# Optimization experiments

Hardware: AMD Instinct MI355X
Metric: run time of the kernel (lower is better)

Reference implementation:

```python
import jax, jax.numpy as jnp
import numpy as np

N = 25000      # nodes
E = 400000     # edges (avg degree 16)
D = 128        # input feature dim
H = 4          # heads in layer 1
O1 = 128       # per-head out dim layer 1
O2 = 64        # out dim layer 2 (1 head)
NG = 512       # number of graphs in batch
NEG_SLOPE = 0.2


def _gat_layer(x, src, dst, W, a_src, a_dst, bias, heads, out_dim):
    """PyG-style GATConv: gather, per-edge logits, segment softmax over dst, scatter-add."""
    n = x.shape[0]
    h = (x @ W).reshape(n, heads, out_dim)              # [N,H,O]
    al_s = jnp.sum(h * a_src, axis=-1)                  # [N,H]
    al_d = jnp.sum(h * a_dst, axis=-1)                  # [N,H]
    e = jax.nn.leaky_relu(al_s[src] + al_d[dst], NEG_SLOPE)   # [E,H]
    e_max = jax.ops.segment_max(e, dst, num_segments=n)        # [N,H]
    e_exp = jnp.exp(e - e_max[dst])
    denom = jax.ops.segment_sum(e_exp, dst, num_segments=n)    # [N,H]
    alpha = e_exp / denom[dst]                                  # [E,H]
    msg = alpha[:, :, None] * h[src]                             # [E,H,O]  (dominant traffic)
    out = jax.ops.segment_sum(msg, dst, num_segments=n)         # [N,H,O]
    return out.reshape(n, heads * out_dim) + bias


def setup_inputs() -> dict:
    key = jax.random.key(0)
    ks = jax.random.split(key, 16)
    x = jax.random.normal(ks[0], (N, D), dtype=jnp.float32)
    edge_index = jax.random.randint(ks[1], (2, E), 0, N, dtype=jnp.int64)
    batch = jnp.sort(jax.random.randint(ks[2], (N,), 0, NG, dtype=jnp.int64))
    def glorot(k, shape, fan_in):
        return jax.random.normal(k, shape, dtype=jnp.float32) * (1.0 / np.sqrt(fan_in))
    W1 = glorot(ks[3], (D, H * O1), D)
    a_src1 = glorot(ks[4], (H, O1), O1)
    a_dst1 = glorot(ks[5], (H, O1), O1)
    b1 = jnp.zeros((H * O1,), dtype=jnp.float32)
    W2 = glorot(ks[6], (H * O1, O2), H * O1)
    a_src2 = glorot(ks[7], (1, O2), O2)
    a_dst2 = glorot(ks[8], (1, O2), O2)
    b2 = jnp.zeros((O2,), dtype=jnp.float32)
    fc_w1 = glorot(ks[9], (O2, 32), O2)
    fc_b1 = jnp.zeros((32,), dtype=jnp.float32)
    fc_w2 = glorot(ks[10], (32, 1), 32)
    fc_b2 = jnp.zeros((1,), dtype=jnp.float32)
    return {"x": x, "edge_index": edge_index, "batch": batch,
            "W1": W1, "a_src1": a_src1, "a_dst1": a_dst1, "b1": b1,
            "W2": W2, "a_src2": a_src2, "a_dst2": a_dst2, "b2": b2,
            "fc_w1": fc_w1, "fc_b1": fc_b1, "fc_w2": fc_w2, "fc_b2": fc_b2}


def reference(x, edge_index, batch, W1, a_src1, a_dst1, b1, W2, a_src2, a_dst2, b2,
              fc_w1, fc_b1, fc_w2, fc_b2):
    n = x.shape[0]
    loop = jnp.arange(n, dtype=edge_index.dtype)
    src = jnp.concatenate([edge_index[0], loop])   # add_self_loops=True (PyG default)
    dst = jnp.concatenate([edge_index[1], loop])
    h1 = jax.nn.elu(_gat_layer(x, src, dst, W1, a_src1, a_dst1, b1, H, O1))   # [N, 512]
    h2 = jax.nn.elu(_gat_layer(h1, src, dst, W2, a_src2, a_dst2, b2, 1, O2))  # [N, 64]
    # global mean pool over graphs
    sums = jax.ops.segment_sum(h2, batch, num_segments=NG)                     # [NG, 64]
    cnt = jax.ops.segment_sum(jnp.ones((n,), dtype=h2.dtype), batch, num_segments=NG)
    pooled = sums / jnp.maximum(cnt, 1.0)[:, None]
    hid = jax.nn.relu(pooled @ fc_w1 + fc_b1)
    out = jax.nn.sigmoid(hid @ fc_w2 + fc_b2)
    return out.squeeze(-1)                                                     # [NG]
```

## Files before the change

kernel.cpp:

```cpp
#include <hip/hip_runtime.h>
#include <hip/hip_bf16.h>


typedef unsigned short u16;
typedef unsigned int u32;
typedef __attribute__((ext_vector_type(8))) short bf16x8;
typedef __attribute__((ext_vector_type(4))) float f32x4;

#define LRELU(v) ((v) > 0.0f ? (v) : 0.2f * (v))
#define ELU(v)   ((v) > 0.0f ? (v) : expm1f(v))

__device__ __forceinline__ u16 f2bf(float f) {
    union { float f; u32 u; } c; c.f = f;
    u32 u = c.u;
    u32 r = (u + 0x7fffu + ((u >> 16) & 1u)) >> 16;
    return (u16)r;
}
__device__ __forceinline__ float bf2f(u16 h) {
    return __uint_as_float(((u32)h) << 16);
}

__global__ __launch_bounds__(256) void prep_w(const float* __restrict__ W1,
                                              const float* __restrict__ W2,
                                              const float* __restrict__ a_s,
                                              const float* __restrict__ a_d,
                                              u16* __restrict__ W1f,
                                              u16* __restrict__ W2f,
                                              float* __restrict__ Wa) {
    int b = blockIdx.x;
    if (b < 384) {
        int idx = b * 256 + threadIdx.x;
        if (idx < 65536) {
            int fid = idx >> 9, l = (idx >> 3) & 63, j = idx & 7;
            int head = fid >> 5, cb = (fid >> 2) & 7, s = fid & 3;
            int col = head * 128 + cb * 16 + (l & 15);
            int k = s * 32 + 16 * (j >> 2) + 4 * (l >> 4) + (j & 3);
            W1f[idx] = f2bf(W1[(size_t)k * 512 + col]);
        } else {
            int i2 = idx - 65536;
            int fid = i2 >> 9, l = (i2 >> 3) & 63, j = i2 & 7;
            int c2 = fid >> 4, s = fid & 15;
            int col = c2 * 16 + (l & 15);
            int k = s * 32 + 16 * (j >> 2) + 4 * (l >> 4) + (j & 3);
            W2f[i2] = f2bf(W2[(size_t)k * 64 + col]);
        }
    } else {
        int idx = (b - 384) * 256 + threadIdx.x;
        int k = idx >> 3, j = idx & 7, h = j & 3;
        const float* a = (j < 4) ? (a_s + h * 128) : (a_d + h * 128);
        const float* wrow = W1 + (size_t)k * 512 + h * 128;
        float s = 0.f;
#pragma unroll 8
        for (int o = 0; o < 128; ++o) s += wrow[o] * a[o];
        Wa[k * 8 + j] = s;
    }
}

__global__ __launch_bounds__(256) void prep_x(const float* __restrict__ x,
                                              const float* __restrict__ Wa,
                                              u16* __restrict__ xbf,
                                              float* __restrict__ alS,
                                              float* __restrict__ alD, int Nn) {
    int lane = threadIdx.x & 63;
    int wave = threadIdx.x >> 6;
    float4 ls = *(const float4*)(Wa + lane * 8);
    float4 ld = *(const float4*)(Wa + lane * 8 + 4);
    float4 hs = *(const float4*)(Wa + (lane + 64) * 8);
    float4 hd = *(const float4*)(Wa + (lane + 64) * 8 + 4);
    int n = blockIdx.x * 4 + wave;
    if (n >= Nn) return;
    float x0 = x[(size_t)n * 128 + lane];
    float x1 = x[(size_t)n * 128 + lane + 64];
    xbf[(size_t)n * 128 + lane]      = f2bf(x0);
    xbf[(size_t)n * 128 + lane + 64] = f2bf(x1);
    float r0 = x0 * ls.x + x1 * hs.x;
    float r1 = x0 * ls.y + x1 * hs.y;
    float r2 = x0 * ls.z + x1 * hs.z;
    float r3 = x0 * ls.w + x1 * hs.w;
    float r4 = x0 * ld.x + x1 * hd.x;
    float r5 = x0 * ld.y + x1 * hd.y;
    float r6 = x0 * ld.z + x1 * hd.z;
    float r7 = x0 * ld.w + x1 * hd.w;
#pragma unroll
    for (int off = 32; off; off >>= 1) {
        r0 += __shfl_down(r0, off); r1 += __shfl_down(r1, off);
        r2 += __shfl_down(r2, off); r3 += __shfl_down(r3, off);
        r4 += __shfl_down(r4, off); r5 += __shfl_down(r5, off);
        r6 += __shfl_down(r6, off); r7 += __shfl_down(r7, off);
    }
    if (lane == 0) {
        *(float4*)(alS + (size_t)n * 4) = make_float4(r0, r1, r2, r3);
        *(float4*)(alD + (size_t)n * 4) = make_float4(r4, r5, r6, r7);
    }
}

__global__ __launch_bounds__(256) void count_kernel(const int* __restrict__ dst,
                                                    int E, int Nn, int* __restrict__ deg) {
    int e = blockIdx.x * 256 + threadIdx.x;
    if (e >= E + Nn) return;
    int d = (e < E) ? dst[e] : (e - E);
    atomicAdd(&deg[d], 1);
}

__global__ __launch_bounds__(256) void scanA_kernel(const int* __restrict__ deg,
                                                    int* __restrict__ offs,
                                                    int* __restrict__ bsum, int n) {
    __shared__ int sh[256];
    int b = blockIdx.x, t = threadIdx.x;
    int base = b * 2048 + t * 8;
    int v[8]; int s = 0;
#pragma unroll
    for (int j = 0; j < 8; ++j) { int i = base + j; v[j] = (i < n) ? deg[i] : 0; s += v[j]; }
    sh[t] = s;
    __syncthreads();
    for (int off = 1; off < 256; off <<= 1) {
        int u = (t >= off) ? sh[t - off] : 0;
        __syncthreads();
        sh[t] += u;
        __syncthreads();
    }
    int run = sh[t] - s;
    if (t == 255) bsum[b] = sh[255];
#pragma unroll
    for (int j = 0; j < 8; ++j) {
        run += v[j];
        int i = base + j;
        if (i < n) offs[i + 1] = run;
    }
}

__global__ __launch_bounds__(64) void scanB_kernel(int* __restrict__ bsum, int nb) {
    int t = threadIdx.x;
    int v = (t < nb) ? bsum[t] : 0;
#pragma unroll
    for (int off = 1; off < 64; off <<= 1) {
        int u = __shfl_up(v, off);
        if (t >= off) v += u;
    }
    if (t < nb) bsum[t] = v;
}

__global__ __launch_bounds__(256) void scanC_kernel(int* __restrict__ offs,
                                                    const int* __restrict__ bsum, int n) {
    int i = blockIdx.x * 256 + threadIdx.x;
    if (i == 0) offs[0] = 0;
    if (i >= n) return;
    int b = i >> 11;
    if (b > 0) offs[i + 1] += bsum[b - 1];
}

__global__ __launch_bounds__(256) void scatter_kernel(const int* __restrict__ src,
                                                      const int* __restrict__ dst,
                                                      int E, int Nn,
                                                      const int* __restrict__ offs,
                                                      int* __restrict__ fill,
                                                      const float* __restrict__ alS,
                                                      const float* __restrict__ alD,
                                                      int* __restrict__ sCSR,
                                                      int* __restrict__ dCSR,
                                                      float* __restrict__ wE1) {
    int e = blockIdx.x * 256 + threadIdx.x;
    if (e >= E + Nn) return;
    int s = (e < E) ? src[e] : (e - E);
    int d = (e < E) ? dst[e] : (e - E);
    int pos = offs[d] + atomicAdd(&fill[d], 1);
    sCSR[pos] = s;
    dCSR[pos] = d;
    float4 as = *(const float4*)(alS + (size_t)s * 4);
    float4 ad = *(const float4*)(alD + (size_t)d * 4);
    float4 w;
    float t;
    t = as.x + ad.x; w.x = expf(LRELU(t));
    t = as.y + ad.y; w.y = expf(LRELU(t));
    t = as.z + ad.z; w.z = expf(LRELU(t));
    t = as.w + ad.w; w.w = expf(LRELU(t));
    *(float4*)(wE1 + (size_t)pos * 4) = w;
}

__global__ __launch_bounds__(256) void aggx_kernel(const u16* __restrict__ xbf,
                                                   const int* __restrict__ sCSR,
                                                   const int* __restrict__ offs,
                                                   const float* __restrict__ wE,
                                                   u16* __restrict__ xaggF, int Nn) {
    int n = blockIdx.x * 4 + (threadIdx.x >> 6);
    int l = threadIdx.x & 63;
    if (n >= Nn) return;
    int half = l >> 5;
    int fl = (l & 31) * 4;
    float a0[4] = {0.f, 0.f, 0.f, 0.f};
    float a1[4] = {0.f, 0.f, 0.f, 0.f};
    float a2[4] = {0.f, 0.f, 0.f, 0.f};
    float a3[4] = {0.f, 0.f, 0.f, 0.f};
    float ws0 = 0.f, ws1 = 0.f, ws2 = 0.f, ws3 = 0.f;
    int s0 = offs[n], s1 = offs[n + 1];
    int i = s0 + half;
    for (; i + 6 < s1; i += 8) {
        int sn[4]; float4 w[4]; ushort4 u[4];
#pragma unroll
        for (int j = 0; j < 4; ++j) {
            int idx = i + 2 * j;
            sn[j] = sCSR[idx];
            w[j] = *(const float4*)(wE + (size_t)idx * 4);
        }
#pragma unroll
        for (int j = 0; j < 4; ++j)
            u[j] = *(const ushort4*)(xbf + (size_t)sn[j] * 128 + fl);
#pragma unroll
        for (int j = 0; j < 4; ++j) {
            float xv[4] = {bf2f(u[j].x), bf2f(u[j].y), bf2f(u[j].z), bf2f(u[j].w)};
#pragma unroll
            for (int q = 0; q < 4; ++q) {
                a0[q] += w[j].x * xv[q];
                a1[q] += w[j].y * xv[q];
                a2[q] += w[j].z * xv[q];
                a3[q] += w[j].w * xv[q];
            }
            ws0 += w[j].x; ws1 += w[j].y; ws2 += w[j].z; ws3 += w[j].w;
        }
    }
    for (; i < s1; i += 2) {
        int sn = sCSR[i];
        float4 w = *(const float4*)(wE + (size_t)i * 4);
        ushort4 u = *(const ushort4*)(xbf + (size_t)sn * 128 + fl);
        float xv[4] = {bf2f(u.x), bf2f(u.y), bf2f(u.z), bf2f(u.w)};
#pragma unroll
        for (int q = 0; q < 4; ++q) {
            a0[q] += w.x * xv[q];
            a1[q] += w.y * xv[q];
            a2[q] += w.z * xv[q];
            a3[q] += w.w * xv[q];
        }
        ws0 += w.x; ws1 += w.y; ws2 += w.z; ws3 += w.w;
    }
#pragma unroll
    for (int q = 0; q < 4; ++q) {
        a0[q] += __shfl_xor(a0[q], 32);
        a1[q] += __shfl_xor(a1[q], 32);
        a2[q] += __shfl_xor(a2[q], 32);
        a3[q] += __shfl_xor(a3[q], 32);
    }
    ws0 += __shfl_xor(ws0, 32); ws1 += __shfl_xor(ws1, 32);
    ws2 += __shfl_xor(ws2, 32); ws3 += __shfl_xor(ws3, 32);
    if (half == 0) {
        float i0 = 1.f / ws0, i1 = 1.f / ws1, i2 = 1.f / ws2, i3 = 1.f / ws3;
        int group = n >> 4, lrow = n & 15;
        int sl = fl >> 5;
        int kg = (fl >> 2) & 3;
        int j0 = ((fl >> 4) & 1) * 4;
        size_t base = ((size_t)group * 16 + sl) * 512 + (size_t)(kg * 16 + lrow) * 8 + j0;
        ushort4 o;
        o.x = f2bf(a0[0] * i0); o.y = f2bf(a0[1] * i0);
        o.z = f2bf(a0[2] * i0); o.w = f2bf(a0[3] * i0);
        *(ushort4*)(xaggF + base + 0 * 2048) = o;
        o.x = f2bf(a1[0] * i1); o.y = f2bf(a1[1] * i1);
        o.z = f2bf(a1[2] * i1); o.w = f2bf(a1[3] * i1);
        *(ushort4*)(xaggF + base + 1 * 2048) = o;
        o.x = f2bf(a2[0] * i2); o.y = f2bf(a2[1] * i2);
        o.z = f2bf(a2[2] * i2); o.w = f2bf(a2[3] * i2);
        *(ushort4*)(xaggF + base + 2 * 2048) = o;
        o.x = f2bf(a3[0] * i3); o.y = f2bf(a3[1] * i3);
        o.z = f2bf(a3[2] * i3); o.w = f2bf(a3[3] * i3);
        *(ushort4*)(xaggF + base + 3 * 2048) = o;
    }
}

__global__ __launch_bounds__(64) void gemm1_mfma(const u16* __restrict__ xaggF,
                                                 const u16* __restrict__ W1f,
                                                 const float* __restrict__ b1,
                                                 u16* __restrict__ out1F) {
    int l = threadIdx.x;
    int head = blockIdx.y;
    int g0 = blockIdx.x * 2;
    int kg = l >> 4;

    bf16x8 xf[2][4];
#pragma unroll
    for (int g = 0; g < 2; ++g) {
        const u16* p = xaggF + ((size_t)(g0 + g) * 16 + head * 4) * 512 + l * 8;
#pragma unroll
        for (int s = 0; s < 4; ++s) xf[g][s] = *(const bf16x8*)(p + s * 512);
    }

    const u16* wbase = W1f + (size_t)head * 32 * 512 + l * 8;

#pragma unroll
    for (int cbp = 0; cbp < 4; ++cbp) {
        bf16x8 op0, op1;
#pragma unroll
        for (int par = 0; par < 2; ++par) {
            int cb = cbp * 2 + par;
            bf16x8 wf[4];
#pragma unroll
            for (int s = 0; s < 4; ++s)
                wf[s] = *(const bf16x8*)(wbase + (size_t)(cb * 4 + s) * 512);
            float4 bias = *(const float4*)(b1 + head * 128 + cb * 16 + kg * 4);
#pragma unroll
            for (int g = 0; g < 2; ++g) {
                f32x4 acc = {0.f, 0.f, 0.f, 0.f};
#pragma unroll
                for (int s = 0; s < 4; ++s)
                    acc = __builtin_amdgcn_mfma_f32_16x16x32_bf16(wf[s], xf[g][s],
                                                                  acc, 0, 0, 0);
                float v0 = ELU(acc[0] + bias.x);
                float v1 = ELU(acc[1] + bias.y);
                float v2 = ELU(acc[2] + bias.z);
                float v3 = ELU(acc[3] + bias.w);
                bf16x8& op = g ? op1 : op0;
                if (par == 0) {
                    op[0] = (short)f2bf(v0); op[1] = (short)f2bf(v1);
                    op[2] = (short)f2bf(v2); op[3] = (short)f2bf(v3);
                } else {
                    op[4] = (short)f2bf(v0); op[5] = (short)f2bf(v1);
                    op[6] = (short)f2bf(v2); op[7] = (short)f2bf(v3);
                }
            }
        }
#pragma unroll
        for (int g = 0; g < 2; ++g) {
            u16* op = out1F + ((size_t)(g0 + g) * 16 + head * 4 + cbp) * 512 + l * 8;
            *(bf16x8*)op = g ? op1 : op0;
        }
    }
}

__global__ __launch_bounds__(64) void gemm2_mfma(const u16* __restrict__ out1F,
                                                 const u16* __restrict__ W2f,
                                                 const float* __restrict__ a_s2,
                                                 const float* __restrict__ a_d2,
                                                 u16* __restrict__ h2bf,
                                                 float* __restrict__ alS,
                                                 float* __restrict__ alD, int M) {
    int l = threadIdx.x;
    int g = blockIdx.x;
    int lrow = l & 15, kg = l >> 4;
    int node = g * 16 + lrow;

    const u16* xp = out1F + (size_t)g * 16 * 512 + l * 8;
    bf16x8 xf[16];
#pragma unroll
    for (int s = 0; s < 16; ++s) xf[s] = *(const bf16x8*)(xp + s * 512);

    const u16* wp = W2f + l * 8;
    float ps = 0.f, pd = 0.f;
#pragma unroll
    for (int c2 = 0; c2 < 4; ++c2) {
        int c0 = c2 * 16;
        f32x4 acc = {0.f, 0.f, 0.f, 0.f};
#pragma unroll
        for (int s = 0; s < 16; ++s) {
            bf16x8 wf = *(const bf16x8*)(wp + (size_t)(c2 * 16 + s) * 512);
            acc = __builtin_amdgcn_mfma_f32_16x16x32_bf16(wf, xf[s], acc, 0, 0, 0);
        }
        float4 as = *(const float4*)(a_s2 + c0 + kg * 4);
        float4 ad = *(const float4*)(a_d2 + c0 + kg * 4);
        ps += acc[0] * as.x + acc[1] * as.y + acc[2] * as.z + acc[3] * as.w;
        pd += acc[0] * ad.x + acc[1] * ad.y + acc[2] * ad.z + acc[3] * ad.w;
        if (node < M) {
            ushort4 o;
            o.x = f2bf(acc[0]); o.y = f2bf(acc[1]);
            o.z = f2bf(acc[2]); o.w = f2bf(acc[3]);
            *(ushort4*)(h2bf + (size_t)node * 64 + c0 + kg * 4) = o;
        }
    }
    ps += __shfl_xor(ps, 16); ps += __shfl_xor(ps, 32);
    pd += __shfl_xor(pd, 16); pd += __shfl_xor(pd, 32);
    if (kg == 0 && node < M) { alS[node] = ps; alD[node] = pd; }
}

__global__ __launch_bounds__(256) void edgew2_kernel(const int* __restrict__ sCSR,
                                                     const int* __restrict__ dCSR,
                                                     int Et,
                                                     const float* __restrict__ alS,
                                                     const float* __restrict__ alD,
                                                     float* __restrict__ wE) {
    int i = blockIdx.x * 256 + threadIdx.x;
    if (i >= Et) return;
    int s = sCSR[i], d = dCSR[i];
    float t = alS[s] + alD[d];
    wE[i] = expf(LRELU(t));
}

__global__ __launch_bounds__(256) void agg2_kernel(const u16* __restrict__ h2bf,
                                                   const int* __restrict__ sCSR,
                                                   const int* __restrict__ offs,
                                                   const float* __restrict__ wE,
                                                   const float* __restrict__ b2,
                                                   float* __restrict__ out2, int Nn) {
    int n = blockIdx.x * 4 + (threadIdx.x >> 6);
    int l = threadIdx.x & 63;
    if (n >= Nn) return;
    int half = l >> 5;
    int fl = (l & 31) * 2;
    float ax = 0.f, ay = 0.f, ws = 0.f;
    int s0 = offs[n], s1 = offs[n + 1];
    int i = s0 + half;
    for (; i + 6 < s1; i += 8) {
        int sn[4]; float w[4]; u32 u[4];
#pragma unroll
        for (int j = 0; j < 4; ++j) {
            int idx = i + 2 * j;
            sn[j] = sCSR[idx];
            w[j] = wE[idx];
        }
#pragma unroll
        for (int j = 0; j < 4; ++j)
            u[j] = *(const u32*)(h2bf + (size_t)sn[j] * 64 + fl);
#pragma unroll
        for (int j = 0; j < 4; ++j) {
            ax += w[j] * __uint_as_float(u[j] << 16);
            ay += w[j] * __uint_as_float(u[j] & 0xffff0000u);
            ws += w[j];
        }
    }
    for (; i < s1; i += 2) {
        int sn = sCSR[i];
        float w = wE[i];
        u32 u = *(const u32*)(h2bf + (size_t)sn * 64 + fl);
        ax += w * __uint_as_float(u << 16);
        ay += w * __uint_as_float(u & 0xffff0000u);
        ws += w;
    }
    ax += __shfl_xor(ax, 32);
    ay += __shfl_xor(ay, 32);
    ws += __shfl_xor(ws, 32);
    if (half == 0) {
        float inv = 1.f / ws;
        float2 o;
        float v0 = ax * inv + b2[fl];
        float v1 = ay * inv + b2[fl + 1];
        o.x = ELU(v0);
        o.y = ELU(v1);
        *(float2*)(out2 + (size_t)n * 64 + fl) = o;
    }
}

__device__ __forceinline__ int lower_bound_i(const int* arr, int n, int key) {
    int lo = 0, hi = n;
    while (lo < hi) {
        int mid = (lo + hi) >> 1;
        if (arr[mid] < key) lo = mid + 1; else hi = mid;
    }
    return lo;
}

__global__ __launch_bounds__(64) void poolfc_kernel(const float* __restrict__ h2,
                                                    const int* __restrict__ batch,
                                                    int Nn,
                                                    const float* __restrict__ w1,
                                                    const float* __restrict__ bb1,
                                                    const float* __restrict__ w2,
                                                    const float* __restrict__ bb2,
                                                    float* __restrict__ out) {
    int g = blockIdx.x;
    __shared__ int sh[2];
    __shared__ float p[64];
    __shared__ float hid[32];
    int t = threadIdx.x;
    if (t == 0) sh[0] = lower_bound_i(batch, Nn, g);
    if (t == 1) sh[1] = lower_bound_i(batch, Nn, g + 1);
    __syncthreads();
    int s0 = sh[0], s1 = sh[1];
    float sum = 0.f;
    for (int i = s0; i < s1; ++i) sum += h2[(size_t)i * 64 + t];
    float cnt = (float)((s1 - s0) > 1 ? (s1 - s0) : 1);
    p[t] = sum / cnt;
    __syncthreads();
    if (t < 32) {
        float a = bb1[t];
#pragma unroll
        for (int k = 0; k < 64; ++k) a += p[k] * w1[k * 32 + t];
        hid[t] = a > 0.f ? a : 0.f;
    }
    __syncthreads();
    if (t == 0) {
        float a = bb2[0];
#pragma unroll
        for (int j = 0; j < 32; ++j) a += hid[j] * w2[j];
        out[g] = 1.0f / (1.0f + expf(-a));
    }
}

extern "C" void kernel_launch(void* const* d_in, const int* in_sizes, int n_in,
                              void* d_out, int out_size, void* d_ws, size_t ws_size,
                              hipStream_t stream) {
    const float* x      = (const float*)d_in[0];
    const int*   ei     = (const int*)d_in[1];
    const int*   batch  = (const int*)d_in[2];
    const float* W1     = (const float*)d_in[3];
    const float* a_src1 = (const float*)d_in[4];
    const float* a_dst1 = (const float*)d_in[5];
    const float* b1     = (const float*)d_in[6];
    const float* W2     = (const float*)d_in[7];
    const float* a_src2 = (const float*)d_in[8];
    const float* a_dst2 = (const float*)d_in[9];
    const float* b2     = (const float*)d_in[10];
    const float* fcw1   = (const float*)d_in[11];
    const float* fcb1   = (const float*)d_in[12];
    const float* fcw2   = (const float*)d_in[13];
    const float* fcb2   = (const float*)d_in[14];
    float* out = (float*)d_out;

    const int Nn = in_sizes[0] / 128;
    const int E  = in_sizes[1] / 2;
    const int Et = E + Nn;
    const int NG = out_size;
    const int* srcA = ei;
    const int* dstA = ei + E;

    const int ngroups = (Nn + 15) / 16;
    const int ngp = (ngroups + 1) & ~1;

    char* base = (char*)d_ws;
    size_t off = 0;
    auto alloc = [&](size_t bytes) -> void* {
        void* p = base + off;
        off += (bytes + 255) & ~(size_t)255;
        return p;
    };
    u16*   xbf    = (u16*)alloc((size_t)Nn * 128 * 2);
    u16*   xaggF  = (u16*)alloc((size_t)ngp * 16 * 512 * 2);
    u16*   out1F  = (u16*)alloc((size_t)ngp * 16 * 512 * 2);
    u16*   h2bf   = (u16*)alloc((size_t)Nn * 64 * 2);
    float* out2   = (float*)alloc((size_t)Nn * 64 * 4);
    u16*   W1f    = (u16*)alloc(65536 * 2);
    u16*   W2f    = (u16*)alloc(32768 * 2);
    float* Wa     = (float*)alloc(128 * 8 * 4);
    float* alS1   = (float*)alloc((size_t)Nn * 4 * 4);
    float* alD1   = (float*)alloc((size_t)Nn * 4 * 4);
    float* alS2   = (float*)alloc((size_t)Nn * 4);
    float* alD2   = (float*)alloc((size_t)Nn * 4);
    float* wE1    = (float*)alloc((size_t)Et * 4 * 4);
    float* wE2    = (float*)alloc((size_t)Et * 4);
    int*   deg    = (int*)alloc((size_t)2 * Nn * 4);
    int*   fill   = deg + Nn;
    int*   offs   = (int*)alloc((size_t)(Nn + 1) * 4);
    int*   bsum   = (int*)alloc(64 * 4);
    int*   sCSR   = (int*)alloc((size_t)Et * 4);
    int*   dCSR   = (int*)alloc((size_t)Et * 4);
    (void)ws_size; (void)n_in;

    const int EB = (Et + 255) / 256;
    const int NB = (Nn + 2047) / 2048;

    prep_w<<<388, 256, 0, stream>>>(W1, W2, a_src1, a_dst1, W1f, W2f, Wa);
    prep_x<<<(Nn + 3) / 4, 256, 0, stream>>>(x, Wa, xbf, alS1, alD1, Nn);

    hipMemsetAsync(deg, 0, sizeof(int) * 2 * Nn, stream);
    count_kernel<<<EB, 256, 0, stream>>>(dstA, E, Nn, deg);
    scanA_kernel<<<NB, 256, 0, stream>>>(deg, offs, bsum, Nn);
    scanB_kernel<<<1, 64, 0, stream>>>(bsum, NB);
    scanC_kernel<<<(Nn + 255) / 256, 256, 0, stream>>>(offs, bsum, Nn);
    scatter_kernel<<<EB, 256, 0, stream>>>(srcA, dstA, E, Nn, offs, fill,
                                           alS1, alD1, sCSR, dCSR, wE1);

    aggx_kernel<<<(Nn + 3) / 4, 256, 0, stream>>>(xbf, sCSR, offs, wE1, xaggF, Nn);
    dim3 g1(ngp / 2, 4);
    gemm1_mfma<<<g1, 64, 0, stream>>>(xaggF, W1f, b1, out1F);

    gemm2_mfma<<<ngroups, 64, 0, stream>>>(out1F, W2f, a_src2, a_dst2,
                                           h2bf, alS2, alD2, Nn);
    edgew2_kernel<<<EB, 256, 0, stream>>>(sCSR, dCSR, Et, alS2, alD2, wE2);
    agg2_kernel<<<(Nn + 3) / 4, 256, 0, stream>>>(h2bf, sCSR, offs, wE2, b2, out2, Nn);

    poolfc_kernel<<<NG, 64, 0, stream>>>(out2, batch, Nn, fcw1, fcb1, fcw2, fcb2, out);
}
```

Before: 189.9 us.

## Compute edge attention weights on the fly and fuse small preprocessing launches

Edge attention weights for both layers are now recomputed inside the aggregation kernels from per-node logits, instead of being written to per-edge wE1/wE2 buffers in scatter and edgew2. This removes the edgew2 kernel and the dCSR array. Degree zeroing moves into prep_w and degree counting into prep_x as extra blocks, and scanB is dropped by having scanC sum the block totals serially. Together these cut kernel launches and per-edge memory traffic, at the cost of repeating exp evaluations and gathering alS per neighbour inside the aggregation loops.

```diff
diff --git a/kernel.cpp b/kernel.cpp
--- a/kernel.cpp
+++ b/kernel.cpp
@@ -26,7 +26,8 @@
                                               const float* __restrict__ a_d,
                                               u16* __restrict__ W1f,
                                               u16* __restrict__ W2f,
-                                              float* __restrict__ Wa) {
+                                              float* __restrict__ Wa,
+                                              int* __restrict__ deg, int nDeg) {
     int b = blockIdx.x;
     if (b < 384) {
         int idx = b * 256 + threadIdx.x;
@@ -44,7 +45,7 @@
             int k = s * 32 + 16 * (j >> 2) + 4 * (l >> 4) + (j & 3);
             W2f[i2] = f2bf(W2[(size_t)k * 64 + col]);
         }
-    } else {
+    } else if (b < 388) {
         int idx = (b - 384) * 256 + threadIdx.x;
         int k = idx >> 3, j = idx & 7, h = j & 3;
         const float* a = (j < 4) ? (a_s + h * 128) : (a_d + h * 128);
@@ -53,21 +54,36 @@
 #pragma unroll 8
         for (int o = 0; o < 128; ++o) s += wrow[o] * a[o];
         Wa[k * 8 + j] = s;
+    } else {
+        int i = (b - 388) * 1024 + threadIdx.x * 4;
+        if (i < nDeg) *(int4*)(deg + i) = make_int4(0, 0, 0, 0);
     }
 }
 
 __global__ __launch_bounds__(256) void prep_x(const float* __restrict__ x,
                                               const float* __restrict__ Wa,
+                                              const int* __restrict__ dstA,
                                               u16* __restrict__ xbf,
                                               float* __restrict__ alS,
-                                              float* __restrict__ alD, int Nn) {
+                                              float* __restrict__ alD,
+                                              int* __restrict__ deg,
+                                              int Nn, int E, int NBx) {
+    int b = blockIdx.x;
+    if (b >= NBx) {
+        int e = (b - NBx) * 256 + threadIdx.x;
+        if (e < E + Nn) {
+            int d = (e < E) ? dstA[e] : (e - E);
+            atomicAdd(&deg[d], 1);
+        }
+        return;
+    }
     int lane = threadIdx.x & 63;
     int wave = threadIdx.x >> 6;
     float4 ls = *(const float4*)(Wa + lane * 8);
     float4 ld = *(const float4*)(Wa + lane * 8 + 4);
     float4 hs = *(const float4*)(Wa + (lane + 64) * 8);
     float4 hd = *(const float4*)(Wa + (lane + 64) * 8 + 4);
-    int n = blockIdx.x * 4 + wave;
+    int n = b * 4 + wave;
     if (n >= Nn) return;
     float x0 = x[(size_t)n * 128 + lane];
     float x1 = x[(size_t)n * 128 + lane + 64];
@@ -94,14 +110,6 @@
     }
 }
 
-__global__ __launch_bounds__(256) void count_kernel(const int* __restrict__ dst,
-                                                    int E, int Nn, int* __restrict__ deg) {
-    int e = blockIdx.x * 256 + threadIdx.x;
-    if (e >= E + Nn) return;
-    int d = (e < E) ? dst[e] : (e - E);
-    atomicAdd(&deg[d], 1);
-}
-
 __global__ __launch_bounds__(256) void scanA_kernel(const int* __restrict__ deg,
                                                     int* __restrict__ offs,
                                                     int* __restrict__ bsum, int n) {
@@ -129,24 +137,15 @@
     }
 }
 
-__global__ __launch_bounds__(64) void scanB_kernel(int* __restrict__ bsum, int nb) {
-    int t = threadIdx.x;
-    int v = (t < nb) ? bsum[t] : 0;
-#pragma unroll
-    for (int off = 1; off < 64; off <<= 1) {
-        int u = __shfl_up(v, off);
-        if (t >= off) v += u;
-    }
-    if (t < nb) bsum[t] = v;
-}
-
 __global__ __launch_bounds__(256) void scanC_kernel(int* __restrict__ offs,
                                                     const int* __restrict__ bsum, int n) {
     int i = blockIdx.x * 256 + threadIdx.x;
     if (i == 0) offs[0] = 0;
     if (i >= n) return;
     int b = i >> 11;
-    if (b > 0) offs[i + 1] += bsum[b - 1];
+    int add = 0;
+    for (int j = 0; j < b; ++j) add += bsum[j];
+    if (b > 0) offs[i + 1] += add;
 }
 
 __global__ __launch_bounds__(256) void scatter_kernel(const int* __restrict__ src,
@@ -154,39 +153,27 @@
                                                       int E, int Nn,
                                                       const int* __restrict__ offs,
                                                       int* __restrict__ fill,
-                                                      const float* __restrict__ alS,
-                                                      const float* __restrict__ alD,
-                                                      int* __restrict__ sCSR,
-                                                      int* __restrict__ dCSR,
-                                                      float* __restrict__ wE1) {
+                                                      int* __restrict__ sCSR) {
     int e = blockIdx.x * 256 + threadIdx.x;
     if (e >= E + Nn) return;
     int s = (e < E) ? src[e] : (e - E);
     int d = (e < E) ? dst[e] : (e - E);
     int pos = offs[d] + atomicAdd(&fill[d], 1);
     sCSR[pos] = s;
-    dCSR[pos] = d;
-    float4 as = *(const float4*)(alS + (size_t)s * 4);
-    float4 ad = *(const float4*)(alD + (size_t)d * 4);
-    float4 w;
-    float t;
-    t = as.x + ad.x; w.x = expf(LRELU(t));
-    t = as.y + ad.y; w.y = expf(LRELU(t));
-    t = as.z + ad.z; w.z = expf(LRELU(t));
-    t = as.w + ad.w; w.w = expf(LRELU(t));
-    *(float4*)(wE1 + (size_t)pos * 4) = w;
 }
 
 __global__ __launch_bounds__(256) void aggx_kernel(const u16* __restrict__ xbf,
                                                    const int* __restrict__ sCSR,
                                                    const int* __restrict__ offs,
-                                                   const float* __restrict__ wE,
+                                                   const float* __restrict__ alS1,
+                                                   const float* __restrict__ alD1,
                                                    u16* __restrict__ xaggF, int Nn) {
     int n = blockIdx.x * 4 + (threadIdx.x >> 6);
     int l = threadIdx.x & 63;
     if (n >= Nn) return;
     int half = l >> 5;
     int fl = (l & 31) * 4;
+    float4 adv = *(const float4*)(alD1 + (size_t)n * 4);
     float a0[4] = {0.f, 0.f, 0.f, 0.f};
     float a1[4] = {0.f, 0.f, 0.f, 0.f};
     float a2[4] = {0.f, 0.f, 0.f, 0.f};
@@ -195,42 +182,48 @@
     int s0 = offs[n], s1 = offs[n + 1];
     int i = s0 + half;
     for (; i + 6 < s1; i += 8) {
-        int sn[4]; float4 w[4]; ushort4 u[4];
+        int sn[4]; float4 as[4]; ushort4 u[4];
+#pragma unroll
+        for (int j = 0; j < 4; ++j) sn[j] = sCSR[i + 2 * j];
 #pragma unroll
         for (int j = 0; j < 4; ++j) {
-            int idx = i + 2 * j;
-            sn[j] = sCSR[idx];
-            w[j] = *(const float4*)(wE + (size_t)idx * 4);
-        }
-#pragma unroll
-        for (int j = 0; j < 4; ++j)
+            as[j] = *(const float4*)(alS1 + (size_t)sn[j] * 4);
             u[j] = *(const ushort4*)(xbf + (size_t)sn[j] * 128 + fl);
+        }
 #pragma unroll
         for (int j = 0; j < 4; ++j) {
+            float t0 = as[j].x + adv.x; float w0 = expf(LRELU(t0));
+            float t1 = as[j].y + adv.y; float w1 = expf(LRELU(t1));
+            float t2 = as[j].z + adv.z; float w2 = expf(LRELU(t2));
+            float t3 = as[j].w + adv.w; float w3 = expf(LRELU(t3));
             float xv[4] = {bf2f(u[j].x), bf2f(u[j].y), bf2f(u[j].z), bf2f(u[j].w)};
 #pragma unroll
             for (int q = 0; q < 4; ++q) {
-                a0[q] += w[j].x * xv[q];
-                a1[q] += w[j].y * xv[q];
-                a2[q] += w[j].z * xv[q];
-                a3[q] += w[j].w * xv[q];
+                a0[q] += w0 * xv[q];
+                a1[q] += w1 * xv[q];
+                a2[q] += w2 * xv[q];
+                a3[q] += w3 * xv[q];
             }
-            ws0 += w[j].x; ws1 += w[j].y; ws2 += w[j].z; ws3 += w[j].w;
+            ws0 += w0; ws1 += w1; ws2 += w2; ws3 += w3;
         }
     }
     for (; i < s1; i += 2) {
         int sn = sCSR[i];
-        float4 w = *(const float4*)(wE + (size_t)i * 4);
+        float4 as = *(const float4*)(alS1 + (size_t)sn * 4);
         ushort4 u = *(const ushort4*)(xbf + (size_t)sn * 128 + fl);
+        float t0 = as.x + adv.x; float w0 = expf(LRELU(t0));
+        float t1 = as.y + adv.y; float w1 = expf(LRELU(t1));
+        float t2 = as.z + adv.z; float w2 = expf(LRELU(t2));
+        float t3 = as.w + adv.w; float w3 = expf(LRELU(t3));
         float xv[4] = {bf2f(u.x), bf2f(u.y), bf2f(u.z), bf2f(u.w)};
 #pragma unroll
         for (int q = 0; q < 4; ++q) {
-            a0[q] += w.x * xv[q];
-            a1[q] += w.y * xv[q];
-            a2[q] += w.z * xv[q];
-            a3[q] += w.w * xv[q];
-        }
-        ws0 += w.x; ws1 += w.y; ws2 += w.z; ws3 += w.w;
+            a0[q] += w0 * xv[q];
+            a1[q] += w1 * xv[q];
+            a2[q] += w2 * xv[q];
+            a3[q] += w3 * xv[q];
+        }
+        ws0 += w0; ws1 += w1; ws2 += w2; ws3 += w3;
     }
 #pragma unroll
     for (int q = 0; q < 4; ++q) {
@@ -367,23 +360,11 @@
     if (kg == 0 && node < M) { alS[node] = ps; alD[node] = pd; }
 }
 
-__global__ __launch_bounds__(256) void edgew2_kernel(const int* __restrict__ sCSR,
-                                                     const int* __restrict__ dCSR,
-                                                     int Et,
-                                                     const float* __restrict__ alS,
-                                                     const float* __restrict__ alD,
-                                                     float* __restrict__ wE) {
-    int i = blockIdx.x * 256 + threadIdx.x;
-    if (i >= Et) return;
-    int s = sCSR[i], d = dCSR[i];
-    float t = alS[s] + alD[d];
-    wE[i] = expf(LRELU(t));
-}
-
 __global__ __launch_bounds__(256) void agg2_kernel(const u16* __restrict__ h2bf,
                                                    const int* __restrict__ sCSR,
                                                    const int* __restrict__ offs,
-                                                   const float* __restrict__ wE,
+                                                   const float* __restrict__ alS2,
+                                                   const float* __restrict__ alD2,
                                                    const float* __restrict__ b2,
                                                    float* __restrict__ out2, int Nn) {
     int n = blockIdx.x * 4 + (threadIdx.x >> 6);
@@ -391,30 +372,32 @@
     if (n >= Nn) return;
     int half = l >> 5;
     int fl = (l & 31) * 2;
+    float ad = alD2[n];
     float ax = 0.f, ay = 0.f, ws = 0.f;
     int s0 = offs[n], s1 = offs[n + 1];
     int i = s0 + half;
     for (; i + 6 < s1; i += 8) {
-        int sn[4]; float w[4]; u32 u[4];
+        int sn[4]; float als[4]; u32 u[4];
+#pragma unroll
+        for (int j = 0; j < 4; ++j) sn[j] = sCSR[i + 2 * j];
 #pragma unroll
         for (int j = 0; j < 4; ++j) {
-            int idx = i + 2 * j;
-            sn[j] = sCSR[idx];
-            w[j] = wE[idx];
-        }
-#pragma unroll
-        for (int j = 0; j < 4; ++j)
+            als[j] = alS2[sn[j]];
             u[j] = *(const u32*)(h2bf + (size_t)sn[j] * 64 + fl);
+        }
 #pragma unroll
         for (int j = 0; j < 4; ++j) {
-            ax += w[j] * __uint_as_float(u[j] << 16);
-            ay += w[j] * __uint_as_float(u[j] & 0xffff0000u);
-            ws += w[j];
+            float t = als[j] + ad;
+            float w = expf(LRELU(t));
+            ax += w * __uint_as_float(u[j] << 16);
+            ay += w * __uint_as_float(u[j] & 0xffff0000u);
+            ws += w;
         }
     }
     for (; i < s1; i += 2) {
         int sn = sCSR[i];
-        float w = wE[i];
+        float t = alS2[sn] + ad;
+        float w = expf(LRELU(t));
         u32 u = *(const u32*)(h2bf + (size_t)sn * 64 + fl);
         ax += w * __uint_as_float(u << 16);
         ay += w * __uint_as_float(u & 0xffff0000u);
@@ -529,38 +512,35 @@
     float* alD1   = (float*)alloc((size_t)Nn * 4 * 4);
     float* alS2   = (float*)alloc((size_t)Nn * 4);
     float* alD2   = (float*)alloc((size_t)Nn * 4);
-    float* wE1    = (float*)alloc((size_t)Et * 4 * 4);
-    float* wE2    = (float*)alloc((size_t)Et * 4);
     int*   deg    = (int*)alloc((size_t)2 * Nn * 4);
     int*   fill   = deg + Nn;
     int*   offs   = (int*)alloc((size_t)(Nn + 1) * 4);
     int*   bsum   = (int*)alloc(64 * 4);
     int*   sCSR   = (int*)alloc((size_t)Et * 4);
-    int*   dCSR   = (int*)alloc((size_t)Et * 4);
     (void)ws_size; (void)n_in;
 
     const int EB = (Et + 255) / 256;
     const int NB = (Nn + 2047) / 2048;
-
-    prep_w<<<388, 256, 0, stream>>>(W1, W2, a_src1, a_dst1, W1f, W2f, Wa);
-    prep_x<<<(Nn + 3) / 4, 256, 0, stream>>>(x, Wa, xbf, alS1, alD1, Nn);
-
-    hipMemsetAsync(deg, 0, sizeof(int) * 2 * Nn, stream);
-    count_kernel<<<EB, 256, 0, stream>>>(dstA, E, Nn, deg);
+    const int NBx = (Nn + 3) / 4;
+    const int ZB = (2 * Nn + 1023) / 1024;
+
+    prep_w<<<388 + ZB, 256, 0, stream>>>(W1, W2, a_src1, a_dst1, W1f, W2f, Wa,
+                                         deg, 2 * Nn);
+    prep_x<<<NBx + EB, 256, 0, stream>>>(x, Wa, dstA, xbf, alS1, alD1, deg,
+                                         Nn, E, NBx);
     scanA_kernel<<<NB, 256, 0, stream>>>(deg, offs, bsum, Nn);
-    scanB_kernel<<<1, 64, 0, stream>>>(bsum, NB);
     scanC_kernel<<<(Nn + 255) / 256, 256, 0, stream>>>(offs, bsum, Nn);
-    scatter_kernel<<<EB, 256, 0, stream>>>(srcA, dstA, E, Nn, offs, fill,
-                                           alS1, alD1, sCSR, dCSR, wE1);
-
-    aggx_kernel<<<(Nn + 3) / 4, 256, 0, stream>>>(xbf, sCSR, offs, wE1, xaggF, Nn);
+    scatter_kernel<<<EB, 256, 0, stream>>>(srcA, dstA, E, Nn, offs, fill, sCSR);
+
+    aggx_kernel<<<(Nn + 3) / 4, 256, 0, stream>>>(xbf, sCSR, offs, alS1, alD1,
+                                                  xaggF, Nn);
     dim3 g1(ngp / 2, 4);
     gemm1_mfma<<<g1, 64, 0, stream>>>(xaggF, W1f, b1, out1F);
-
     gemm2_mfma<<<ngroups, 64, 0, stream>>>(out1F, W2f, a_src2, a_dst2,
                                            h2bf, alS2, alD2, Nn);
-    edgew2_kernel<<<EB, 256, 0, stream>>>(sCSR, dCSR, Et, alS2, alD2, wE2);
-    agg2_kernel<<<(Nn + 3) / 4, 256, 0, stream>>>(h2bf, sCSR, offs, wE2, b2, out2, Nn);
+
+    agg2_kernel<<<(Nn + 3) / 4, 256, 0, stream>>>(h2bf, sCSR, offs, alS2, alD2,
+                                                  b2, out2, Nn);
 
     poolfc_kernel<<<NG, 64, 0, stream>>>(out2, batch, Nn, fcw1, fcb1, fcw2, fcb2, out);
 }
```

Result: slower. 198.0 us (+4.3%).
